# Optimization experiments

Hardware: AMD Instinct MI355X
Metric: run time of the kernel (lower is better)

Reference implementation:

```python
import jax, jax.numpy as jnp
import numpy as np

B, S, D = 16, 4096, 128
FACTOR = 1


def setup_inputs() -> dict:
    key = jax.random.key(0)
    kq, kk, kv = jax.random.split(key, 3)
    Q = jax.random.normal(kq, (B, S, D), dtype=jnp.float32)
    K = jax.random.normal(kk, (B, S, D), dtype=jnp.float32)
    V = jax.random.normal(kv, (B, S, D), dtype=jnp.float32)
    return {"Q": Q, "K": K, "V": V}


def reference(Q, K, V):
    # [B, S, D] -> [B, D, S] (head dim of 1 is elided; all ops are per-(b,d) lane)
    Qc = jnp.transpose(Q, (0, 2, 1))
    Kc = jnp.transpose(K, (0, 2, 1))
    Vc = jnp.transpose(V, (0, 2, 1))
    seq_len = Qc.shape[-1]
    # FFT cross-correlation: corr[b,d,tau] = sum_t Q[b,d,t] K[b,d,t-tau] (circular)
    corr = jnp.fft.irfft(
        jnp.fft.rfft(Qc, axis=-1) * jnp.conj(jnp.fft.rfft(Kc, axis=-1)),
        n=seq_len, axis=-1)  # [B, D, S]
    top_k = int(FACTOR * np.log(seq_len))  # = 8 for S=4096
    weights, delay = jax.lax.top_k(corr, top_k)  # [B, D, K], raw corr values (no softmax)
    # time-delay aggregation: roll V circularly by each selected delay and weighted-sum
    t = jnp.arange(seq_len)
    idx = (delay[..., None] + t[None, None, None, :]) % seq_len  # [B, D, K, S]
    pattern = jnp.take_along_axis(Vc[:, :, None, :], idx, axis=-1)  # [B, D, K, S]
    out = jnp.einsum('bdks,bdk->bds', pattern, weights)  # [B, D, S]
    # dropout is identity at inference
    return jnp.transpose(out, (0, 2, 1))  # [B, S, D]
```

## Files before the change

kernel.cpp:

```cpp
#include <hip/hip_runtime.h>
#include <math.h>

#define SEQ 4096
#define LOG2SEQ 12
#define TOPK 8
#define NB 16
#define ND 128
#define NEGINF (-3.402823466e+38f)

#define PADF(i) ((i) + ((i) >> 5))

__device__ __forceinline__ int rev12(int x) {
    return (int)(__brev((unsigned)x) >> (32 - LOG2SEQ));
}

__device__ __forceinline__ void transpose_body(const float* __restrict__ inb,
                                               float* __restrict__ outb,
                                               int R, int C) {
    __shared__ float tile[32][33];
    const int c0 = blockIdx.x * 32, r0 = blockIdx.y * 32;
#pragma unroll
    for (int j = 0; j < 32; j += 8) {
        tile[threadIdx.y + j][threadIdx.x] =
            inb[(size_t)(r0 + threadIdx.y + j) * C + (c0 + threadIdx.x)];
    }
    __syncthreads();
#pragma unroll
    for (int j = 0; j < 32; j += 8) {
        outb[(size_t)(c0 + threadIdx.y + j) * R + (r0 + threadIdx.x)] =
            tile[threadIdx.x][threadIdx.y + j];
    }
}

__global__ __launch_bounds__(256) void transpose3_k(const float* __restrict__ Q,
                                                    const float* __restrict__ K,
                                                    const float* __restrict__ V,
                                                    float* __restrict__ Qt,
                                                    float* __restrict__ Kt,
                                                    float* __restrict__ Vt) {
    const int which = blockIdx.z / NB;
    const int b = blockIdx.z % NB;
    const size_t bo = (size_t)b * SEQ * ND;
    const float* in = (which == 0) ? Q : (which == 1) ? K : V;
    float* out = (which == 0) ? Qt : (which == 1) ? Kt : Vt;
    transpose_body(in + bo, out + bo, SEQ, ND);
}

__global__ __launch_bounds__(256) void transpose_back_k(const float* __restrict__ in,
                                                        float* __restrict__ out) {
    const size_t bo = (size_t)blockIdx.z * SEQ * ND;
    transpose_body(in + bo, out + bo, ND, SEQ);
}

__global__ __launch_bounds__(256) void corr_topk_agg_k(const float* Qt,
                                                       const float* __restrict__ Kt,
                                                       const float* __restrict__ Vt,
                                                       float* Ot) {
    __shared__ float re[SEQ + SEQ / 32];
    __shared__ float im[SEQ + SEQ / 32];
    __shared__ float twc[SEQ / 2 + SEQ / 64];
    __shared__ float tws[SEQ / 2 + SEQ / 64];
    __shared__ float sval[4];
    __shared__ int sidx[4];
    __shared__ float wsel[TOPK];
    __shared__ int dsel[TOPK];

    const int tid = threadIdx.x;
    const size_t row = (size_t)blockIdx.x * SEQ;

    for (int j = tid; j < SEQ / 2; j += 256) {
        float s, c;
        sincosf(-6.283185307179586f * (float)j / (float)SEQ, &s, &c);
        twc[PADF(j)] = c;
        tws[PADF(j)] = s;
    }

    {
        const float4* Q4 = (const float4*)(Qt + row);
        const float4* K4 = (const float4*)(Kt + row);
        for (int t = tid; t < SEQ / 4; t += 256) {
            const float4 q = Q4[t];
            const float4 k = K4[t];
            const int b0 = PADF(4 * t);
            re[b0] = q.x; re[b0 + 1] = q.y; re[b0 + 2] = q.z; re[b0 + 3] = q.w;
            im[b0] = k.x; im[b0 + 1] = k.y; im[b0 + 2] = k.z; im[b0 + 3] = k.w;
        }
    }
    __syncthreads();

    for (int h = 2048; h >= 2; h >>= 2) {
        const int hh = h >> 1;
        const int sA = SEQ / (2 * h);
        for (int g = tid; g < SEQ / 4; g += 256) {
            const int pos = g & (hh - 1);
            const int i0 = ((g - pos) << 2) + pos;
            const int p0 = PADF(i0), p1 = PADF(i0 + hh);
            const int p2 = PADF(i0 + h), p3 = PADF(i0 + h + hh);
            const float e0r = re[p0], e0i = im[p0];
            const float e1r = re[p1], e1i = im[p1];
            const float e2r = re[p2], e2i = im[p2];
            const float e3r = re[p3], e3i = im[p3];
            const int ta = pos * sA;
            const int pta = PADF(ta), ptb = PADF(2 * ta);
            const float c1 = twc[pta], s1 = tws[pta];
            const float cB = twc[ptb], sB = tws[ptb];
            const float f0r = e0r + e2r, f0i = e0i + e2i;
            float dr = e0r - e2r, di = e0i - e2i;
            const float f2r = dr * c1 - di * s1, f2i = dr * s1 + di * c1;
            const float f1r = e1r + e3r, f1i = e1i + e3i;
            dr = e1r - e3r;
            di = e1i - e3i;
            const float f3r = dr * s1 + di * c1;
            const float f3i = di * s1 - dr * c1;
            re[p0] = f0r + f1r;
            im[p0] = f0i + f1i;
            dr = f0r - f1r;
            di = f0i - f1i;
            re[p1] = dr * cB - di * sB;
            im[p1] = dr * sB + di * cB;
            re[p2] = f2r + f3r;
            im[p2] = f2i + f3i;
            dr = f2r - f3r;
            di = f2i - f3i;
            re[p3] = dr * cB - di * sB;
            im[p3] = dr * sB + di * cB;
        }
        __syncthreads();
    }

    float ar_[9], ai_[9], br_[9], bi_[9];
#pragma unroll
    for (int q = 0; q < 9; ++q) {
        const int f = tid + (q << 8);
        if (f <= SEQ / 2) {
            const int pa = PADF(rev12(f));
            const int pb = PADF(rev12((SEQ - f) & (SEQ - 1)));
            ar_[q] = re[pa];
            ai_[q] = im[pa];
            br_[q] = re[pb];
            bi_[q] = im[pb];
        }
    }
    __syncthreads();
#pragma unroll
    for (int q = 0; q < 9; ++q) {
        const int f = tid + (q << 8);
        if (f <= SEQ / 2) {
            const float ar = ar_[q], ai = ai_[q], br = br_[q], bi = bi_[q];
            const float Qr = 0.5f * (ar + br), Qi = 0.5f * (ai - bi);
            const float Kr = 0.5f * (ai + bi), Ki = 0.5f * (br - ar);
            const float invS = 1.0f / (float)SEQ;
            const float Pr = (Qr * Kr + Qi * Ki) * invS;
            const float Pi = (Qi * Kr - Qr * Ki) * invS;
            const int pa = PADF(rev12(f));
            const int pb = PADF(rev12((SEQ - f) & (SEQ - 1)));
            re[pa] = Pr;
            im[pa] = Pi;
            re[pb] = Pr;
            im[pb] = -Pi;
        }
    }
    __syncthreads();

    for (int hh = 1; hh <= 1024; hh <<= 2) {
        const int sA = SEQ / (2 * hh);
        const int sB = SEQ / (4 * hh);
        for (int g = tid; g < SEQ / 4; g += 256) {
            const int pos = g & (hh - 1);
            const int i0 = ((g - pos) << 2) + pos;
            const int p0 = PADF(i0), p1 = PADF(i0 + hh);
            const int p2 = PADF(i0 + 2 * hh), p3 = PADF(i0 + 3 * hh);
            const float e0r = re[p0], e0i = im[p0];
            const float e1r = re[p1], e1i = im[p1];
            const float e2r = re[p2], e2i = im[p2];
            const float e3r = re[p3], e3i = im[p3];
            const int pta = PADF(pos * sA), ptb = PADF(pos * sB);
            const float cA = twc[pta], sAv = -tws[pta];
            const float cB = twc[ptb], sBv = -tws[ptb];
            float tr = e1r * cA - e1i * sAv, ti = e1r * sAv + e1i * cA;
            const float f0r = e0r + tr, f0i = e0i + ti;
            const float f1r = e0r - tr, f1i = e0i - ti;
            tr = e3r * cA - e3i * sAv;
            ti = e3r * sAv + e3i * cA;
            const float f2r = e2r + tr, f2i = e2i + ti;
            const float f3r = e2r - tr, f3i = e2i - ti;
            tr = f2r * cB - f2i * sBv;
            ti = f2r * sBv + f2i * cB;
            re[p0] = f0r + tr;
            im[p0] = f0i + ti;
            re[p2] = f0r - tr;
            im[p2] = f0i - ti;
            tr = -f3r * sBv - f3i * cB;
            ti = f3r * cB - f3i * sBv;
            re[p1] = f1r + tr;
            im[p1] = f1i + ti;
            re[p3] = f1r - tr;
            im[p3] = f1i - ti;
        }
        __syncthreads();
    }

    {
        const float4* V4 = (const float4*)(Vt + row);
        for (int t = tid; t < SEQ / 4; t += 256) {
            const float4 v = V4[t];
            const int b0 = PADF(4 * t);
            im[b0] = v.x; im[b0 + 1] = v.y; im[b0 + 2] = v.z; im[b0 + 3] = v.w;
        }
    }

    for (int it = 0; it < TOPK; ++it) {
        float best = NEGINF;
        int bidx = 0;
#pragma unroll
        for (int j = 0; j < SEQ / 256; ++j) {
            const int t = tid + (j << 8);
            const float v = re[PADF(t)];
            if (v > best) {
                best = v;
                bidx = t;
            }
        }
#pragma unroll
        for (int off = 32; off > 0; off >>= 1) {
            const float ov = __shfl_down(best, off);
            const int oi = __shfl_down(bidx, off);
            if (ov > best || (ov == best && oi < bidx)) {
                best = ov;
                bidx = oi;
            }
        }
        if ((tid & 63) == 0) {
            sval[tid >> 6] = best;
            sidx[tid >> 6] = bidx;
        }
        __syncthreads();
        if (tid == 0) {
            float bv = sval[0];
            int bi2 = sidx[0];
#pragma unroll
            for (int w = 1; w < 4; ++w) {
                const float ov = sval[w];
                const int oi = sidx[w];
                if (ov > bv || (ov == bv && oi < bi2)) {
                    bv = ov;
                    bi2 = oi;
                }
            }
            wsel[it] = bv;
            dsel[it] = bi2;
            re[PADF(bi2)] = NEGINF;
        }
        __syncthreads();
    }

    float w[TOPK];
    int dl[TOPK];
#pragma unroll
    for (int k = 0; k < TOPK; ++k) {
        w[k] = wsel[k];
        dl[k] = dsel[k];
    }
    for (int j = 0; j < SEQ / 256; ++j) {
        const int t = tid + (j << 8);
        float acc = 0.0f;
#pragma unroll
        for (int k = 0; k < TOPK; ++k) {
            acc += w[k] * im[PADF((t + dl[k]) & (SEQ - 1))];
        }
        Ot[row + t] = acc;
    }
}

extern "C" void kernel_launch(void* const* d_in, const int* in_sizes, int n_in,
                              void* d_out, int out_size, void* d_ws, size_t ws_size,
                              hipStream_t stream) {
    const float* Q = (const float*)d_in[0];
    const float* K = (const float*)d_in[1];
    const float* V = (const float*)d_in[2];
    float* out = (float*)d_out;

    const size_t n = (size_t)NB * ND * SEQ;
    float* Qt = (float*)d_ws;
    float* Kt = Qt + n;
    float* Vt = Kt + n;

    dim3 tb(32, 8, 1);

    dim3 g1(ND / 32, SEQ / 32, 3 * NB);
    hipLaunchKernelGGL(transpose3_k, g1, tb, 0, stream, Q, K, V, Qt, Kt, Vt);

    hipLaunchKernelGGL(corr_topk_agg_k, dim3(NB * ND), dim3(256), 0, stream,
                       Qt, Kt, Vt, Qt);

    dim3 g3(SEQ / 32, ND / 32, NB);
    hipLaunchKernelGGL(transpose_back_k, g3, tb, 0, stream, Qt, out);
}
```

Before: 259.0 us.

## Interleave complex FFT data in LDS, widen transposes to 64x64 float4 tiles

Stores the FFT working set as interleaved float2 (re,im) with a new padding scheme so each butterfly does one 64-bit LDS access per element instead of two scalar ones, and packs twiddles as float2. The transposes move to 64x64 tiles with float4 global loads and stores, and V is staged in the freed twiddle buffer. Top-k now keeps correlation values in registers and masks winners locally rather than rescanning LDS each iteration. The costs are extra register pressure from the cached values and possible LDS bank conflicts in the transpose's column writes at pitch 68.

```diff
diff --git a/kernel.cpp b/kernel.cpp
--- a/kernel.cpp
+++ b/kernel.cpp
@@ -8,27 +8,40 @@
 #define ND 128
 #define NEGINF (-3.402823466e+38f)
 
+#define PAD2(i) ((i) + ((i) >> 4))
 #define PADF(i) ((i) + ((i) >> 5))
+
+#define TPITCH 68
 
 __device__ __forceinline__ int rev12(int x) {
     return (int)(__brev((unsigned)x) >> (32 - LOG2SEQ));
 }
 
-__device__ __forceinline__ void transpose_body(const float* __restrict__ inb,
-                                               float* __restrict__ outb,
-                                               int R, int C) {
-    __shared__ float tile[32][33];
-    const int c0 = blockIdx.x * 32, r0 = blockIdx.y * 32;
-#pragma unroll
-    for (int j = 0; j < 32; j += 8) {
-        tile[threadIdx.y + j][threadIdx.x] =
-            inb[(size_t)(r0 + threadIdx.y + j) * C + (c0 + threadIdx.x)];
-    }
-    __syncthreads();
-#pragma unroll
-    for (int j = 0; j < 32; j += 8) {
-        outb[(size_t)(c0 + threadIdx.y + j) * R + (r0 + threadIdx.x)] =
-            tile[threadIdx.x][threadIdx.y + j];
+__device__ __forceinline__ void transpose64_body(const float* __restrict__ inb,
+                                                 float* __restrict__ outb,
+                                                 int R, int C) {
+    __shared__ float lds[64 * TPITCH];
+    const int tid = threadIdx.x;
+    const int c0 = blockIdx.x * 64, r0 = blockIdx.y * 64;
+    const int q = tid & 15;
+    const int rr = tid >> 4;
+#pragma unroll
+    for (int pass = 0; pass < 4; ++pass) {
+        const int r = pass * 16 + rr;
+        const float4 v =
+            *(const float4*)(inb + (size_t)(r0 + r) * C + (c0 + 4 * q));
+        const int base = (4 * q) * TPITCH + r;
+        lds[base] = v.x;
+        lds[base + TPITCH] = v.y;
+        lds[base + 2 * TPITCH] = v.z;
+        lds[base + 3 * TPITCH] = v.w;
+    }
+    __syncthreads();
+#pragma unroll
+    for (int pass = 0; pass < 4; ++pass) {
+        const int c = pass * 16 + rr;
+        const float4 v = *(const float4*)(lds + c * TPITCH + 4 * q);
+        *(float4*)(outb + (size_t)(c0 + c) * R + (r0 + 4 * q)) = v;
     }
 }
 
@@ -43,23 +56,21 @@
     const size_t bo = (size_t)b * SEQ * ND;
     const float* in = (which == 0) ? Q : (which == 1) ? K : V;
     float* out = (which == 0) ? Qt : (which == 1) ? Kt : Vt;
-    transpose_body(in + bo, out + bo, SEQ, ND);
+    transpose64_body(in + bo, out + bo, SEQ, ND);
 }
 
 __global__ __launch_bounds__(256) void transpose_back_k(const float* __restrict__ in,
                                                         float* __restrict__ out) {
     const size_t bo = (size_t)blockIdx.z * SEQ * ND;
-    transpose_body(in + bo, out + bo, ND, SEQ);
+    transpose64_body(in + bo, out + bo, ND, SEQ);
 }
 
 __global__ __launch_bounds__(256) void corr_topk_agg_k(const float* Qt,
                                                        const float* __restrict__ Kt,
                                                        const float* __restrict__ Vt,
                                                        float* Ot) {
-    __shared__ float re[SEQ + SEQ / 32];
-    __shared__ float im[SEQ + SEQ / 32];
-    __shared__ float twc[SEQ / 2 + SEQ / 64];
-    __shared__ float tws[SEQ / 2 + SEQ / 64];
+    __shared__ float2 zz[SEQ + SEQ / 16];
+    __shared__ float2 tw2[SEQ / 2 + SEQ / 32];
     __shared__ float sval[4];
     __shared__ int sidx[4];
     __shared__ float wsel[TOPK];
@@ -71,8 +82,7 @@
     for (int j = tid; j < SEQ / 2; j += 256) {
         float s, c;
         sincosf(-6.283185307179586f * (float)j / (float)SEQ, &s, &c);
-        twc[PADF(j)] = c;
-        tws[PADF(j)] = s;
+        tw2[PAD2(j)] = make_float2(c, s);
     }
 
     {
@@ -81,9 +91,11 @@
         for (int t = tid; t < SEQ / 4; t += 256) {
             const float4 q = Q4[t];
             const float4 k = K4[t];
-            const int b0 = PADF(4 * t);
-            re[b0] = q.x; re[b0 + 1] = q.y; re[b0 + 2] = q.z; re[b0 + 3] = q.w;
-            im[b0] = k.x; im[b0 + 1] = k.y; im[b0 + 2] = k.z; im[b0 + 3] = k.w;
+            const int b0 = PAD2(4 * t);
+            zz[b0] = make_float2(q.x, k.x);
+            zz[b0 + 1] = make_float2(q.y, k.y);
+            zz[b0 + 2] = make_float2(q.z, k.z);
+            zz[b0 + 3] = make_float2(q.w, k.w);
         }
     }
     __syncthreads();
@@ -94,51 +106,39 @@
         for (int g = tid; g < SEQ / 4; g += 256) {
             const int pos = g & (hh - 1);
             const int i0 = ((g - pos) << 2) + pos;
-            const int p0 = PADF(i0), p1 = PADF(i0 + hh);
-            const int p2 = PADF(i0 + h), p3 = PADF(i0 + h + hh);
-            const float e0r = re[p0], e0i = im[p0];
-            const float e1r = re[p1], e1i = im[p1];
-            const float e2r = re[p2], e2i = im[p2];
-            const float e3r = re[p3], e3i = im[p3];
+            const int p0 = PAD2(i0), p1 = PAD2(i0 + hh);
+            const int p2 = PAD2(i0 + h), p3 = PAD2(i0 + h + hh);
+            const float2 e0 = zz[p0], e1 = zz[p1], e2 = zz[p2], e3 = zz[p3];
             const int ta = pos * sA;
-            const int pta = PADF(ta), ptb = PADF(2 * ta);
-            const float c1 = twc[pta], s1 = tws[pta];
-            const float cB = twc[ptb], sB = tws[ptb];
-            const float f0r = e0r + e2r, f0i = e0i + e2i;
-            float dr = e0r - e2r, di = e0i - e2i;
-            const float f2r = dr * c1 - di * s1, f2i = dr * s1 + di * c1;
-            const float f1r = e1r + e3r, f1i = e1i + e3i;
-            dr = e1r - e3r;
-            di = e1i - e3i;
-            const float f3r = dr * s1 + di * c1;
-            const float f3i = di * s1 - dr * c1;
-            re[p0] = f0r + f1r;
-            im[p0] = f0i + f1i;
+            const float2 wA = tw2[PAD2(ta)];
+            const float2 wB = tw2[PAD2(2 * ta)];
+            const float f0r = e0.x + e2.x, f0i = e0.y + e2.y;
+            float dr = e0.x - e2.x, di = e0.y - e2.y;
+            const float f2r = dr * wA.x - di * wA.y, f2i = dr * wA.y + di * wA.x;
+            const float f1r = e1.x + e3.x, f1i = e1.y + e3.y;
+            dr = e1.x - e3.x;
+            di = e1.y - e3.y;
+            const float f3r = dr * wA.y + di * wA.x;
+            const float f3i = di * wA.y - dr * wA.x;
+            zz[p0] = make_float2(f0r + f1r, f0i + f1i);
             dr = f0r - f1r;
             di = f0i - f1i;
-            re[p1] = dr * cB - di * sB;
-            im[p1] = dr * sB + di * cB;
-            re[p2] = f2r + f3r;
-            im[p2] = f2i + f3i;
+            zz[p1] = make_float2(dr * wB.x - di * wB.y, dr * wB.y + di * wB.x);
+            zz[p2] = make_float2(f2r + f3r, f2i + f3i);
             dr = f2r - f3r;
             di = f2i - f3i;
-            re[p3] = dr * cB - di * sB;
-            im[p3] = dr * sB + di * cB;
-        }
-        __syncthreads();
-    }
-
-    float ar_[9], ai_[9], br_[9], bi_[9];
+            zz[p3] = make_float2(dr * wB.x - di * wB.y, dr * wB.y + di * wB.x);
+        }
+        __syncthreads();
+    }
+
+    float2 za_[9], zb_[9];
 #pragma unroll
     for (int q = 0; q < 9; ++q) {
         const int f = tid + (q << 8);
         if (f <= SEQ / 2) {
-            const int pa = PADF(rev12(f));
-            const int pb = PADF(rev12((SEQ - f) & (SEQ - 1)));
-            ar_[q] = re[pa];
-            ai_[q] = im[pa];
-            br_[q] = re[pb];
-            bi_[q] = im[pb];
+            za_[q] = zz[PAD2(rev12(f))];
+            zb_[q] = zz[PAD2(rev12((SEQ - f) & (SEQ - 1)))];
         }
     }
     __syncthreads();
@@ -146,18 +146,15 @@
     for (int q = 0; q < 9; ++q) {
         const int f = tid + (q << 8);
         if (f <= SEQ / 2) {
-            const float ar = ar_[q], ai = ai_[q], br = br_[q], bi = bi_[q];
+            const float ar = za_[q].x, ai = za_[q].y;
+            const float br = zb_[q].x, bi = zb_[q].y;
             const float Qr = 0.5f * (ar + br), Qi = 0.5f * (ai - bi);
             const float Kr = 0.5f * (ai + bi), Ki = 0.5f * (br - ar);
             const float invS = 1.0f / (float)SEQ;
             const float Pr = (Qr * Kr + Qi * Ki) * invS;
             const float Pi = (Qi * Kr - Qr * Ki) * invS;
-            const int pa = PADF(rev12(f));
-            const int pb = PADF(rev12((SEQ - f) & (SEQ - 1)));
-            re[pa] = Pr;
-            im[pa] = Pi;
-            re[pb] = Pr;
-            im[pb] = -Pi;
+            zz[PAD2(rev12(f))] = make_float2(Pr, Pi);
+            zz[PAD2(rev12((SEQ - f) & (SEQ - 1)))] = make_float2(Pr, -Pi);
         }
     }
     __syncthreads();
@@ -168,56 +165,56 @@
         for (int g = tid; g < SEQ / 4; g += 256) {
             const int pos = g & (hh - 1);
             const int i0 = ((g - pos) << 2) + pos;
-            const int p0 = PADF(i0), p1 = PADF(i0 + hh);
-            const int p2 = PADF(i0 + 2 * hh), p3 = PADF(i0 + 3 * hh);
-            const float e0r = re[p0], e0i = im[p0];
-            const float e1r = re[p1], e1i = im[p1];
-            const float e2r = re[p2], e2i = im[p2];
-            const float e3r = re[p3], e3i = im[p3];
-            const int pta = PADF(pos * sA), ptb = PADF(pos * sB);
-            const float cA = twc[pta], sAv = -tws[pta];
-            const float cB = twc[ptb], sBv = -tws[ptb];
-            float tr = e1r * cA - e1i * sAv, ti = e1r * sAv + e1i * cA;
-            const float f0r = e0r + tr, f0i = e0i + ti;
-            const float f1r = e0r - tr, f1i = e0i - ti;
-            tr = e3r * cA - e3i * sAv;
-            ti = e3r * sAv + e3i * cA;
-            const float f2r = e2r + tr, f2i = e2i + ti;
-            const float f3r = e2r - tr, f3i = e2i - ti;
+            const int p0 = PAD2(i0), p1 = PAD2(i0 + hh);
+            const int p2 = PAD2(i0 + 2 * hh), p3 = PAD2(i0 + 3 * hh);
+            const float2 e0 = zz[p0], e1 = zz[p1], e2 = zz[p2], e3 = zz[p3];
+            const float2 wA = tw2[PAD2(pos * sA)];
+            const float2 wB = tw2[PAD2(pos * sB)];
+            const float cA = wA.x, sAv = -wA.y;
+            const float cB = wB.x, sBv = -wB.y;
+            float tr = e1.x * cA - e1.y * sAv, ti = e1.x * sAv + e1.y * cA;
+            const float f0r = e0.x + tr, f0i = e0.y + ti;
+            const float f1r = e0.x - tr, f1i = e0.y - ti;
+            tr = e3.x * cA - e3.y * sAv;
+            ti = e3.x * sAv + e3.y * cA;
+            const float f2r = e2.x + tr, f2i = e2.y + ti;
+            const float f3r = e2.x - tr, f3i = e2.y - ti;
             tr = f2r * cB - f2i * sBv;
             ti = f2r * sBv + f2i * cB;
-            re[p0] = f0r + tr;
-            im[p0] = f0i + ti;
-            re[p2] = f0r - tr;
-            im[p2] = f0i - ti;
+            zz[p0] = make_float2(f0r + tr, f0i + ti);
+            zz[p2] = make_float2(f0r - tr, f0i - ti);
             tr = -f3r * sBv - f3i * cB;
             ti = f3r * cB - f3i * sBv;
-            re[p1] = f1r + tr;
-            im[p1] = f1i + ti;
-            re[p3] = f1r - tr;
-            im[p3] = f1i - ti;
-        }
-        __syncthreads();
-    }
-
+            zz[p1] = make_float2(f1r + tr, f1i + ti);
+            zz[p3] = make_float2(f1r - tr, f1i - ti);
+        }
+        __syncthreads();
+    }
+
+    float* vbuf = reinterpret_cast<float*>(tw2);
     {
         const float4* V4 = (const float4*)(Vt + row);
         for (int t = tid; t < SEQ / 4; t += 256) {
             const float4 v = V4[t];
             const int b0 = PADF(4 * t);
-            im[b0] = v.x; im[b0 + 1] = v.y; im[b0 + 2] = v.z; im[b0 + 3] = v.w;
-        }
-    }
-
+            vbuf[b0] = v.x; vbuf[b0 + 1] = v.y;
+            vbuf[b0 + 2] = v.z; vbuf[b0 + 3] = v.w;
+        }
+    }
+
+    float vals[16];
+#pragma unroll
+    for (int j = 0; j < 16; ++j) {
+        vals[j] = zz[PAD2(tid + (j << 8))].x;
+    }
     for (int it = 0; it < TOPK; ++it) {
         float best = NEGINF;
         int bidx = 0;
 #pragma unroll
-        for (int j = 0; j < SEQ / 256; ++j) {
+        for (int j = 0; j < 16; ++j) {
             const int t = tid + (j << 8);
-            const float v = re[PADF(t)];
-            if (v > best) {
-                best = v;
+            if (vals[j] > best) {
+                best = vals[j];
                 bidx = t;
             }
         }
@@ -249,9 +246,13 @@
             }
             wsel[it] = bv;
             dsel[it] = bi2;
-            re[PADF(bi2)] = NEGINF;
-        }
-        __syncthreads();
+        }
+        __syncthreads();
+        const int win = dsel[it];
+#pragma unroll
+        for (int j = 0; j < 16; ++j) {
+            if (tid + (j << 8) == win) vals[j] = NEGINF;
+        }
     }
 
     float w[TOPK];
@@ -266,7 +267,7 @@
         float acc = 0.0f;
 #pragma unroll
         for (int k = 0; k < TOPK; ++k) {
-            acc += w[k] * im[PADF((t + dl[k]) & (SEQ - 1))];
+            acc += w[k] * vbuf[PADF((t + dl[k]) & (SEQ - 1))];
         }
         Ot[row + t] = acc;
     }
@@ -285,14 +286,12 @@
     float* Kt = Qt + n;
     float* Vt = Kt + n;
 
-    dim3 tb(32, 8, 1);
-
-    dim3 g1(ND / 32, SEQ / 32, 3 * NB);
-    hipLaunchKernelGGL(transpose3_k, g1, tb, 0, stream, Q, K, V, Qt, Kt, Vt);
+    dim3 g1(ND / 64, SEQ / 64, 3 * NB);
+    hipLaunchKernelGGL(transpose3_k, g1, dim3(256), 0, stream, Q, K, V, Qt, Kt, Vt);
 
     hipLaunchKernelGGL(corr_topk_agg_k, dim3(NB * ND), dim3(256), 0, stream,
                        Qt, Kt, Vt, Qt);
 
-    dim3 g3(SEQ / 32, ND / 32, NB);
-    hipLaunchKernelGGL(transpose_back_k, g3, tb, 0, stream, Qt, out);
-}
+    dim3 g3(SEQ / 64, ND / 64, NB);
+    hipLaunchKernelGGL(transpose_back_k, g3, dim3(256), 0, stream, Qt, out);
+}
```

Measured after the change: 265.8 us. 1.03x slower.
